# Optimization experiments

Measured on AMD Instinct MI355X. Metric: run time of the kernel, lower is better.

## Reference

```python
import jax, jax.numpy as jnp
import numpy as np

D_MODEL, D_STATE, EXPAND = 1024, 256, 2
BATCH, SEQ = 8, 2048


def setup_inputs() -> dict:
    key = jax.random.key(0)
    ks = jax.random.split(key, 7)
    s = 0.02
    return {
        "x": jax.random.normal(ks[0], (BATCH, SEQ, D_MODEL), jnp.float32),
        "W_in": jax.random.normal(ks[1], (D_MODEL, D_MODEL * EXPAND), jnp.float32) * s,
        "b_in": jax.random.normal(ks[2], (D_MODEL * EXPAND,), jnp.float32) * s,
        "W_state": jax.random.normal(ks[3], (D_MODEL * EXPAND, D_STATE), jnp.float32) * s,
        "b_state": jax.random.normal(ks[4], (D_STATE,), jnp.float32) * s,
        "W_out": jax.random.normal(ks[5], (D_STATE, D_MODEL), jnp.float32) * s,
        "b_out": jax.random.normal(ks[6], (D_MODEL,), jnp.float32) * s,
        "init_state": jnp.zeros((1, D_STATE), jnp.float32),
    }


def reference(x, W_in, b_in, W_state, b_state, W_out, b_out, init_state):
    # x: [B, T, D]
    x_proj = jax.nn.silu(jnp.einsum("btd,de->bte", x, W_in) + b_in)  # [B,T,2D]
    # state_proj depends only on x_proj, so batch the GEMM over all timesteps
    updates = jnp.einsum("bte,es->bts", x_proj, W_state) + b_state    # [B,T,S]
    updates_t = jnp.swapaxes(updates, 0, 1)                            # [T,B,S]
    state0 = jnp.broadcast_to(init_state, (x.shape[0], init_state.shape[1]))

    def step(state, u):
        new = jax.nn.silu(state + u)
        return new, new

    _, states = jax.lax.scan(step, state0, updates_t)  # [T,B,S]
    out = jnp.einsum("tbs,sd->tbd", states, W_out) + b_out  # [T,B,D]
    return jnp.swapaxes(out, 0, 1)  # [B,T,D]
```

## Files before the change

kernel.cpp:

```cpp
#include <hip/hip_runtime.h>
#include <cstdint>
#include <cstddef>

#define BATCH 8
#define SEQ   2048
#define DM    1024
#define DE    2048
#define DSZ   256
#define MROWS (BATCH*SEQ)
#define MCHUNK 8192

typedef _Float16 f16;
typedef _Float16 f16x4 __attribute__((ext_vector_type(4)));
typedef _Float16 f16x8 __attribute__((ext_vector_type(8)));
typedef float  f32x4  __attribute__((ext_vector_type(4)));

__device__ __forceinline__ void glds16(const void* gp, void* lp) {
  __builtin_amdgcn_global_load_lds(
      (const __attribute__((address_space(1))) void*)gp,
      (__attribute__((address_space(3))) void*)lp, 16, 0, 0);
}

__device__ __forceinline__ float silu_f(float x) {
  return x * __builtin_amdgcn_rcpf(1.0f + __expf(-x));
}

__global__ void split_x_k(const float* __restrict__ in, f16* __restrict__ oh,
                          f16* __restrict__ ol, int n) {
  int i = (blockIdx.x * blockDim.x + threadIdx.x) * 4;
  const int stride = gridDim.x * blockDim.x * 4;
  for (; i < n; i += stride) {
    float4 v = *(const float4*)(in + i);
    f16x4 h, l;
    h[0] = (f16)v.x; l[0] = (f16)(v.x - (float)h[0]);
    h[1] = (f16)v.y; l[1] = (f16)(v.y - (float)h[1]);
    h[2] = (f16)v.z; l[2] = (f16)(v.z - (float)h[2]);
    h[3] = (f16)v.w; l[3] = (f16)(v.w - (float)h[3]);
    *(f16x4*)(oh + i) = h;
    *(f16x4*)(ol + i) = l;
  }
}

__global__ void transpose_split_k(const float* __restrict__ in, f16* __restrict__ oh,
                                  f16* __restrict__ ol, int R, int C) {
  __shared__ float tile[32][33];
  const int c0 = blockIdx.x * 32, r0 = blockIdx.y * 32;
  const int tx = threadIdx.x, ty = threadIdx.y;
  #pragma unroll
  for (int i = 0; i < 4; ++i)
    tile[ty + i*8][tx] = in[(size_t)(r0 + ty + i*8) * C + c0 + tx];
  __syncthreads();
  #pragma unroll
  for (int i = 0; i < 4; ++i) {
    float v = tile[tx][ty + i*8];
    f16 h = (f16)v;
    size_t idx = (size_t)(c0 + ty + i*8) * R + r0 + tx;
    oh[idx] = h;
    ol[idx] = (f16)(v - (float)h);
  }
}

__global__ void transpose_cast_f16_k(const float* __restrict__ in, f16* __restrict__ out, int R, int C) {
  __shared__ float tile[32][33];
  const int c0 = blockIdx.x * 32, r0 = blockIdx.y * 32;
  const int tx = threadIdx.x, ty = threadIdx.y;
  #pragma unroll
  for (int i = 0; i < 4; ++i)
    tile[ty + i*8][tx] = in[(size_t)(r0 + ty + i*8) * C + c0 + tx];
  __syncthreads();
  #pragma unroll
  for (int i = 0; i < 4; ++i)
    out[(size_t)(c0 + ty + i*8) * R + r0 + tx] = (f16)tile[tx][ty + i*8];
}

__global__ __launch_bounds__(512) void gemm1_k(const f16* __restrict__ Ah, const f16* __restrict__ Al,
                                               const f16* __restrict__ Bh, const f16* __restrict__ Bl,
                                               const float* __restrict__ bias,
                                               f16* __restrict__ Ch, f16* __restrict__ Cl) {
  const int K = 1024, N = 2048;
  __shared__ f16 sAh[4096], sAl[4096], sBh[4096], sBl[4096];

  const int tid = threadIdx.x;
  const int w = tid >> 6, l = tid & 63;
  const int bid = blockIdx.x;
  const int xcd = bid & 7, loc = bid >> 3;
  const int mt = xcd * 8 + (loc & 7);
  const int nt = loc >> 3;
  const int bm = mt * 128, bn = nt * 128;
  const int wm = (w >> 2) * 64, wn = (w & 3) * 32;
  const int lr = l & 15, lq = l >> 4;

  const int r = tid >> 2, k8 = tid & 3;
  const f16* pAh = Ah + (size_t)(bm + r) * K + k8 * 8;
  const f16* pAl = Al + (size_t)(bm + r) * K + k8 * 8;
  const f16* pBh = Bh + (size_t)(bn + r) * K + k8 * 8;
  const f16* pBl = Bl + (size_t)(bn + r) * K + k8 * 8;
  f16* dAh = sAh + tid * 8; f16* dAl = sAl + tid * 8;
  f16* dBh = sBh + tid * 8; f16* dBl = sBl + tid * 8;

  int offA[4], offB[2];
  #pragma unroll
  for (int i = 0; i < 4; ++i) offA[i] = (wm + i*16 + lr) * 32 + lq * 8;
  #pragma unroll
  for (int j = 0; j < 2; ++j) offB[j] = (wn + j*16 + lr) * 32 + lq * 8;

  f32x4 acc[4][2] = {};

  for (int kk = 0; kk < K; kk += 32) {
    __syncthreads();
    glds16(pAh, dAh); glds16(pAl, dAl);
    glds16(pBh, dBh); glds16(pBl, dBl);
    pAh += 32; pAl += 32; pBh += 32; pBl += 32;
    asm volatile("s_waitcnt vmcnt(0)" ::: "memory");
    __syncthreads();

    f16x8 ah[4], al[4], bh[2], bl[2];
    #pragma unroll
    for (int i = 0; i < 4; ++i) {
      ah[i] = *(const f16x8*)(sAh + offA[i]);
      al[i] = *(const f16x8*)(sAl + offA[i]);
    }
    #pragma unroll
    for (int j = 0; j < 2; ++j) {
      bh[j] = *(const f16x8*)(sBh + offB[j]);
      bl[j] = *(const f16x8*)(sBl + offB[j]);
    }
    #pragma unroll
    for (int i = 0; i < 4; ++i)
      #pragma unroll
      for (int j = 0; j < 2; ++j) {
        acc[i][j] = __builtin_amdgcn_mfma_f32_16x16x32_f16(ah[i], bh[j], acc[i][j], 0, 0, 0);
        acc[i][j] = __builtin_amdgcn_mfma_f32_16x16x32_f16(ah[i], bl[j], acc[i][j], 0, 0, 0);
        acc[i][j] = __builtin_amdgcn_mfma_f32_16x16x32_f16(al[i], bh[j], acc[i][j], 0, 0, 0);
      }
  }

  #pragma unroll
  for (int j = 0; j < 2; ++j) {
    const int col = bn + wn + j*16 + lr;
    const float bv = bias[col];
    #pragma unroll
    for (int i = 0; i < 4; ++i)
      #pragma unroll
      for (int r4 = 0; r4 < 4; ++r4) {
        const int row = bm + wm + i*16 + lq*4 + r4;
        const float s = silu_f(acc[i][j][r4] + bv);
        const f16 h = (f16)s;
        const size_t idx = (size_t)row * N + col;
        Ch[idx] = h;
        Cl[idx] = (f16)(s - (float)h);
      }
  }
}

__global__ __launch_bounds__(256) void gemm2s_k(const f16* __restrict__ Ah, const f16* __restrict__ Al,
                                                const f16* __restrict__ Bh, const f16* __restrict__ Bl,
                                                const float* __restrict__ bias,
                                                float* __restrict__ C) {
  const int K = 2048, N = 256;
  __shared__ f16 sAh[2048], sAl[2048], sBh[4096], sBl[4096];

  const int tid = threadIdx.x;
  const int w = tid >> 6, l = tid & 63;
  const int bm = blockIdx.y * 64, bn = blockIdx.x * 128;
  const int wm = (w & 1) * 32, wn = (w >> 1) * 64;
  const int lr = l & 15, lq = l >> 4;

  const int rA = tid >> 2, k8 = tid & 3;
  const f16* pAh = Ah + (size_t)(bm + rA) * K + k8 * 8;
  const f16* pAl = Al + (size_t)(bm + rA) * K + k8 * 8;
  f16* dAh = sAh + tid * 8; f16* dAl = sAl + tid * 8;
  const f16 *pBh[2], *pBl[2]; f16 *dBh[2], *dBl[2];
  #pragma unroll
  for (int p = 0; p < 2; ++p) {
    const int c = p * 256 + tid;
    const int rB = c >> 2;
    pBh[p] = Bh + (size_t)(bn + rB) * K + (c & 3) * 8;
    pBl[p] = Bl + (size_t)(bn + rB) * K + (c & 3) * 8;
    dBh[p] = sBh + (size_t)c * 8; dBl[p] = sBl + (size_t)c * 8;
  }

  int offA[2], offB[4];
  #pragma unroll
  for (int i = 0; i < 2; ++i) offA[i] = (wm + i*16 + lr) * 32 + lq * 8;
  #pragma unroll
  for (int j = 0; j < 4; ++j) offB[j] = (wn + j*16 + lr) * 32 + lq * 8;

  f32x4 acc[2][4] = {};

  for (int kk = 0; kk < K; kk += 32) {
    __syncthreads();
    glds16(pAh, dAh); glds16(pAl, dAl);
    pAh += 32; pAl += 32;
    #pragma unroll
    for (int p = 0; p < 2; ++p) {
      glds16(pBh[p], dBh[p]); pBh[p] += 32;
      glds16(pBl[p], dBl[p]); pBl[p] += 32;
    }
    asm volatile("s_waitcnt vmcnt(0)" ::: "memory");
    __syncthreads();

    f16x8 ah[2], al[2], bh[4], bl[4];
    #pragma unroll
    for (int i = 0; i < 2; ++i) {
      ah[i] = *(const f16x8*)(sAh + offA[i]);
      al[i] = *(const f16x8*)(sAl + offA[i]);
    }
    #pragma unroll
    for (int j = 0; j < 4; ++j) {
      bh[j] = *(const f16x8*)(sBh + offB[j]);
      bl[j] = *(const f16x8*)(sBl + offB[j]);
    }
    #pragma unroll
    for (int i = 0; i < 2; ++i)
      #pragma unroll
      for (int j = 0; j < 4; ++j) {
        acc[i][j] = __builtin_amdgcn_mfma_f32_16x16x32_f16(ah[i], bh[j], acc[i][j], 0, 0, 0);
        acc[i][j] = __builtin_amdgcn_mfma_f32_16x16x32_f16(ah[i], bl[j], acc[i][j], 0, 0, 0);
        acc[i][j] = __builtin_amdgcn_mfma_f32_16x16x32_f16(al[i], bh[j], acc[i][j], 0, 0, 0);
      }
  }

  #pragma unroll
  for (int j = 0; j < 4; ++j) {
    const int col = bn + wn + j*16 + lr;
    const float bv = bias[col];
    #pragma unroll
    for (int i = 0; i < 2; ++i)
      #pragma unroll
      for (int r4 = 0; r4 < 4; ++r4) {
        const int row = bm + wm + i*16 + lq*4 + r4;
        C[(size_t)row * N + col] = acc[i][j][r4] + bv;
      }
  }
}

__global__ __launch_bounds__(256) void gemm3_k(const f16* __restrict__ A,
                                               const f16* __restrict__ Bt,
                                               const float* __restrict__ bias,
                                               float* __restrict__ C) {
  const int K = 256, N = 1024;
  __shared__ f16 sA[4096], sB[4096];

  const int tid = threadIdx.x;
  const int w = tid >> 6, l = tid & 63;
  const int bm = blockIdx.y * 128, bn = blockIdx.x * 128;
  const int wm = (w >> 1) * 64, wn = (w & 1) * 64;
  const int lr = l & 15, lq = l >> 4;

  const f16 *pA[2], *pB[2]; f16 *dA[2], *dB[2];
  #pragma unroll
  for (int p = 0; p < 2; ++p) {
    const int c = p * 256 + tid;
    const int r = c >> 2, k8 = c & 3;
    pA[p] = A  + (size_t)(bm + r) * K + k8 * 8;
    pB[p] = Bt + (size_t)(bn + r) * K + k8 * 8;
    dA[p] = sA + (size_t)c * 8;
    dB[p] = sB + (size_t)c * 8;
  }

  int offA[4], offB[4];
  #pragma unroll
  for (int i = 0; i < 4; ++i) {
    offA[i] = (wm + i*16 + lr) * 32 + lq * 8;
    offB[i] = (wn + i*16 + lr) * 32 + lq * 8;
  }

  f32x4 acc[4][4] = {};

  for (int kk = 0; kk < K; kk += 32) {
    __syncthreads();
    glds16(pA[0], dA[0]); glds16(pA[1], dA[1]);
    glds16(pB[0], dB[0]); glds16(pB[1], dB[1]);
    pA[0] += 32; pA[1] += 32; pB[0] += 32; pB[1] += 32;
    asm volatile("s_waitcnt vmcnt(0)" ::: "memory");
    __syncthreads();

    f16x8 af[4], bfr[4];
    #pragma unroll
    for (int i = 0; i < 4; ++i) af[i]  = *(const f16x8*)(sA + offA[i]);
    #pragma unroll
    for (int j = 0; j < 4; ++j) bfr[j] = *(const f16x8*)(sB + offB[j]);
    #pragma unroll
    for (int i = 0; i < 4; ++i)
      #pragma unroll
      for (int j = 0; j < 4; ++j)
        acc[i][j] = __builtin_amdgcn_mfma_f32_16x16x32_f16(af[i], bfr[j], acc[i][j], 0, 0, 0);
  }

  #pragma unroll
  for (int j = 0; j < 4; ++j) {
    const int col = bn + wn + j*16 + lr;
    const float bv = bias[col];
    #pragma unroll
    for (int i = 0; i < 4; ++i)
      #pragma unroll
      for (int r4 = 0; r4 < 4; ++r4) {
        const int row = bm + wm + i*16 + lq*4 + r4;
        C[(size_t)row * N + col] = acc[i][j][r4] + bv;
      }
  }
}

#define L2E 1.4426950408889634f
__global__ void scan_k(const float* __restrict__ upd, const float* __restrict__ init,
                       f16* __restrict__ states) {
  const int b = blockIdx.x, s = threadIdx.x;
  const float* u = upd + (size_t)b * SEQ * DSZ + s;
  f16* st = states + (size_t)b * SEQ * DSZ + s;
  float state = init[s];

  float ucur[16], unext[16], ulog[16];
  #pragma unroll
  for (int i = 0; i < 16; ++i) ucur[i] = u[(size_t)i * DSZ];
  #pragma unroll
  for (int i = 0; i < 16; ++i) ulog[i] = ucur[i] * (-L2E);

  for (int t0 = 0; t0 < SEQ; t0 += 16) {
    if (t0 + 16 < SEQ) {
      #pragma unroll
      for (int i = 0; i < 16; ++i) unext[i] = u[(size_t)(t0 + 16 + i) * DSZ];
    }
    f16 res[16];
    #pragma unroll
    for (int i = 0; i < 16; ++i) {
      const float e = __builtin_amdgcn_exp2f(__builtin_fmaf(state, -L2E, ulog[i]));
      const float x = state + ucur[i];
      state = x * __builtin_amdgcn_rcpf(1.0f + e);
      res[i] = (f16)state;
    }
    #pragma unroll
    for (int i = 0; i < 16; ++i) st[(size_t)(t0 + i) * DSZ] = res[i];
    #pragma unroll
    for (int i = 0; i < 16; ++i) { ucur[i] = unext[i]; ulog[i] = unext[i] * (-L2E); }
  }
}

extern "C" void kernel_launch(void* const* d_in, const int* in_sizes, int n_in,
                              void* d_out, int out_size, void* d_ws, size_t ws_size,
                              hipStream_t stream) {
  const float* x       = (const float*)d_in[0];
  const float* W_in    = (const float*)d_in[1];
  const float* b_in    = (const float*)d_in[2];
  const float* W_state = (const float*)d_in[3];
  const float* b_state = (const float*)d_in[4];
  const float* W_out   = (const float*)d_in[5];
  const float* b_out   = (const float*)d_in[6];
  const float* init_st = (const float*)d_in[7];
  float* out = (float*)d_out;

  char* ws = (char*)d_ws;
  f16*   xh        = (f16*)(ws + 0);
  f16*   xl        = (f16*)(ws + 33554432);
  f16*   xproj_h   = (f16*)(ws + 67108864);
  f16*   xproj_l   = (f16*)(ws + 100663296);
  float* upd       = (float*)(ws + 134217728);
  f16*   states    = (f16*)(ws + 150994944);
  f16*   w_in_h    = (f16*)(ws + 159383552);
  f16*   w_in_l    = (f16*)(ws + 163577856);
  f16*   w_state_h = (f16*)(ws + 167772160);
  f16*   w_state_l = (f16*)(ws + 168820736);
  f16*   w_out_t   = (f16*)(ws + 169869312);

  split_x_k<<<4096, 256, 0, stream>>>(x, xh, xl, MROWS * DM);
  dim3 tb(32, 8);
  transpose_split_k<<<dim3(DE/32,  DM/32), tb, 0, stream>>>(W_in,    w_in_h,    w_in_l,    DM,  DE);
  transpose_split_k<<<dim3(DSZ/32, DE/32), tb, 0, stream>>>(W_state, w_state_h, w_state_l, DE,  DSZ);
  transpose_cast_f16_k<<<dim3(DM/32, DSZ/32), tb, 0, stream>>>(W_out, w_out_t, DSZ, DM);

  for (int c = 0; c < 2; ++c) {
    const size_t ro = (size_t)c * MCHUNK;
    gemm1_k<<<1024, 512, 0, stream>>>(
        xh + ro * DM, xl + ro * DM, w_in_h, w_in_l, b_in, xproj_h, xproj_l);
    gemm2s_k<<<dim3(DSZ/128, MCHUNK/64), 256, 0, stream>>>(
        xproj_h, xproj_l, w_state_h, w_state_l, b_state, upd + ro * DSZ);
  }

  scan_k<<<BATCH, DSZ, 0, stream>>>(upd, init_st, states);

  gemm3_k<<<dim3(DM/128, MROWS/128), 256, 0, stream>>>(states, w_out_t, b_out, out);
}
```

Baseline: 625.4 us.

## Swizzle LDS tiles, shrink gemm2 tile, split scan across more blocks

Applies an XOR swizzle to the k-chunk index of the LDS tiles in all three GEMMs, so fragment reads hit different LDS banks. gemm2s moves from a 64x128 to a 64x64 tile, doubling the grid to raise occupancy. The scan kernel is split into 32 blocks of 64 threads instead of 8 blocks of 256, and now prefetches two chunks ahead to hide load latency. The trade-offs are more registers in the scan and more redundant A-tile reloads in gemm2s.

Result: faster. 592.6 us (-5.2%).

```diff
diff --git a/kernel.cpp b/kernel.cpp
--- a/kernel.cpp
+++ b/kernel.cpp
@@ -24,6 +24,8 @@
 __device__ __forceinline__ float silu_f(float x) {
   return x * __builtin_amdgcn_rcpf(1.0f + __expf(-x));
 }
+
+__device__ __forceinline__ int swz(int k8, int r) { return k8 ^ ((r >> 1) & 3); }
 
 __global__ void split_x_k(const float* __restrict__ in, f16* __restrict__ oh,
                           f16* __restrict__ ol, int n) {
@@ -90,7 +92,7 @@
   const int wm = (w >> 2) * 64, wn = (w & 3) * 32;
   const int lr = l & 15, lq = l >> 4;
 
-  const int r = tid >> 2, k8 = tid & 3;
+  const int r = tid >> 2, k8 = swz(tid & 3, r);
   const f16* pAh = Ah + (size_t)(bm + r) * K + k8 * 8;
   const f16* pAl = Al + (size_t)(bm + r) * K + k8 * 8;
   const f16* pBh = Bh + (size_t)(bn + r) * K + k8 * 8;
@@ -100,9 +102,15 @@
 
   int offA[4], offB[2];
   #pragma unroll
-  for (int i = 0; i < 4; ++i) offA[i] = (wm + i*16 + lr) * 32 + lq * 8;
-  #pragma unroll
-  for (int j = 0; j < 2; ++j) offB[j] = (wn + j*16 + lr) * 32 + lq * 8;
+  for (int i = 0; i < 4; ++i) {
+    const int row = wm + i*16 + lr;
+    offA[i] = row * 32 + swz(lq, row) * 8;
+  }
+  #pragma unroll
+  for (int j = 0; j < 2; ++j) {
+    const int row = wn + j*16 + lr;
+    offB[j] = row * 32 + swz(lq, row) * 8;
+  }
 
   f32x4 acc[4][2] = {};
 
@@ -158,63 +166,59 @@
                                                 const float* __restrict__ bias,
                                                 float* __restrict__ C) {
   const int K = 2048, N = 256;
-  __shared__ f16 sAh[2048], sAl[2048], sBh[4096], sBl[4096];
+  __shared__ f16 sAh[2048], sAl[2048], sBh[2048], sBl[2048];
 
   const int tid = threadIdx.x;
   const int w = tid >> 6, l = tid & 63;
-  const int bm = blockIdx.y * 64, bn = blockIdx.x * 128;
-  const int wm = (w & 1) * 32, wn = (w >> 1) * 64;
+  const int bm = blockIdx.y * 64, bn = blockIdx.x * 64;
+  const int wm = (w & 1) * 32, wn = (w >> 1) * 32;
   const int lr = l & 15, lq = l >> 4;
 
-  const int rA = tid >> 2, k8 = tid & 3;
-  const f16* pAh = Ah + (size_t)(bm + rA) * K + k8 * 8;
-  const f16* pAl = Al + (size_t)(bm + rA) * K + k8 * 8;
+  const int r = tid >> 2, k8 = swz(tid & 3, r);
+  const f16* pAh = Ah + (size_t)(bm + r) * K + k8 * 8;
+  const f16* pAl = Al + (size_t)(bm + r) * K + k8 * 8;
+  const f16* pBh = Bh + (size_t)(bn + r) * K + k8 * 8;
+  const f16* pBl = Bl + (size_t)(bn + r) * K + k8 * 8;
   f16* dAh = sAh + tid * 8; f16* dAl = sAl + tid * 8;
-  const f16 *pBh[2], *pBl[2]; f16 *dBh[2], *dBl[2];
-  #pragma unroll
-  for (int p = 0; p < 2; ++p) {
-    const int c = p * 256 + tid;
-    const int rB = c >> 2;
-    pBh[p] = Bh + (size_t)(bn + rB) * K + (c & 3) * 8;
-    pBl[p] = Bl + (size_t)(bn + rB) * K + (c & 3) * 8;
-    dBh[p] = sBh + (size_t)c * 8; dBl[p] = sBl + (size_t)c * 8;
-  }
-
-  int offA[2], offB[4];
-  #pragma unroll
-  for (int i = 0; i < 2; ++i) offA[i] = (wm + i*16 + lr) * 32 + lq * 8;
-  #pragma unroll
-  for (int j = 0; j < 4; ++j) offB[j] = (wn + j*16 + lr) * 32 + lq * 8;
-
-  f32x4 acc[2][4] = {};
+  f16* dBh = sBh + tid * 8; f16* dBl = sBl + tid * 8;
+
+  int offA[2], offB[2];
+  #pragma unroll
+  for (int i = 0; i < 2; ++i) {
+    const int row = wm + i*16 + lr;
+    offA[i] = row * 32 + swz(lq, row) * 8;
+  }
+  #pragma unroll
+  for (int j = 0; j < 2; ++j) {
+    const int row = wn + j*16 + lr;
+    offB[j] = row * 32 + swz(lq, row) * 8;
+  }
+
+  f32x4 acc[2][2] = {};
 
   for (int kk = 0; kk < K; kk += 32) {
     __syncthreads();
     glds16(pAh, dAh); glds16(pAl, dAl);
-    pAh += 32; pAl += 32;
-    #pragma unroll
-    for (int p = 0; p < 2; ++p) {
-      glds16(pBh[p], dBh[p]); pBh[p] += 32;
-      glds16(pBl[p], dBl[p]); pBl[p] += 32;
-    }
+    glds16(pBh, dBh); glds16(pBl, dBl);
+    pAh += 32; pAl += 32; pBh += 32; pBl += 32;
     asm volatile("s_waitcnt vmcnt(0)" ::: "memory");
     __syncthreads();
 
-    f16x8 ah[2], al[2], bh[4], bl[4];
+    f16x8 ah[2], al[2], bh[2], bl[2];
     #pragma unroll
     for (int i = 0; i < 2; ++i) {
       ah[i] = *(const f16x8*)(sAh + offA[i]);
       al[i] = *(const f16x8*)(sAl + offA[i]);
     }
     #pragma unroll
-    for (int j = 0; j < 4; ++j) {
+    for (int j = 0; j < 2; ++j) {
       bh[j] = *(const f16x8*)(sBh + offB[j]);
       bl[j] = *(const f16x8*)(sBl + offB[j]);
     }
     #pragma unroll
     for (int i = 0; i < 2; ++i)
       #pragma unroll
-      for (int j = 0; j < 4; ++j) {
+      for (int j = 0; j < 2; ++j) {
         acc[i][j] = __builtin_amdgcn_mfma_f32_16x16x32_f16(ah[i], bh[j], acc[i][j], 0, 0, 0);
         acc[i][j] = __builtin_amdgcn_mfma_f32_16x16x32_f16(ah[i], bl[j], acc[i][j], 0, 0, 0);
         acc[i][j] = __builtin_amdgcn_mfma_f32_16x16x32_f16(al[i], bh[j], acc[i][j], 0, 0, 0);
@@ -222,7 +226,7 @@
   }
 
   #pragma unroll
-  for (int j = 0; j < 4; ++j) {
+  for (int j = 0; j < 2; ++j) {
     const int col = bn + wn + j*16 + lr;
     const float bv = bias[col];
     #pragma unroll
@@ -252,7 +256,7 @@
   #pragma unroll
   for (int p = 0; p < 2; ++p) {
     const int c = p * 256 + tid;
-    const int r = c >> 2, k8 = c & 3;
+    const int r = c >> 2, k8 = swz(c & 3, r);
     pA[p] = A  + (size_t)(bm + r) * K + k8 * 8;
     pB[p] = Bt + (size_t)(bn + r) * K + k8 * 8;
     dA[p] = sA + (size_t)c * 8;
@@ -262,8 +266,10 @@
   int offA[4], offB[4];
   #pragma unroll
   for (int i = 0; i < 4; ++i) {
-    offA[i] = (wm + i*16 + lr) * 32 + lq * 8;
-    offB[i] = (wn + i*16 + lr) * 32 + lq * 8;
+    const int rowA = wm + i*16 + lr;
+    const int rowB = wn + i*16 + lr;
+    offA[i] = rowA * 32 + swz(lq, rowA) * 8;
+    offB[i] = rowB * 32 + swz(lq, rowB) * 8;
   }
 
   f32x4 acc[4][4] = {};
@@ -303,36 +309,40 @@
 }
 
 #define L2E 1.4426950408889634f
-__global__ void scan_k(const float* __restrict__ upd, const float* __restrict__ init,
-                       f16* __restrict__ states) {
-  const int b = blockIdx.x, s = threadIdx.x;
+__global__ __launch_bounds__(64) void scan_k(const float* __restrict__ upd,
+                                             const float* __restrict__ init,
+                                             f16* __restrict__ states) {
+  const int b = blockIdx.x >> 2, sq = blockIdx.x & 3;
+  const int s = sq * 64 + threadIdx.x;
   const float* u = upd + (size_t)b * SEQ * DSZ + s;
   f16* st = states + (size_t)b * SEQ * DSZ + s;
   float state = init[s];
 
-  float ucur[16], unext[16], ulog[16];
-  #pragma unroll
-  for (int i = 0; i < 16; ++i) ucur[i] = u[(size_t)i * DSZ];
-  #pragma unroll
-  for (int i = 0; i < 16; ++i) ulog[i] = ucur[i] * (-L2E);
+  float r0[16], r1[16], r2[16], ulog[16];
+  #pragma unroll
+  for (int i = 0; i < 16; ++i) r0[i] = u[(size_t)i * DSZ];
+  #pragma unroll
+  for (int i = 0; i < 16; ++i) r1[i] = u[(size_t)(16 + i) * DSZ];
+  #pragma unroll
+  for (int i = 0; i < 16; ++i) ulog[i] = r0[i] * (-L2E);
 
   for (int t0 = 0; t0 < SEQ; t0 += 16) {
-    if (t0 + 16 < SEQ) {
-      #pragma unroll
-      for (int i = 0; i < 16; ++i) unext[i] = u[(size_t)(t0 + 16 + i) * DSZ];
+    if (t0 + 32 < SEQ) {
+      #pragma unroll
+      for (int i = 0; i < 16; ++i) r2[i] = u[(size_t)(t0 + 32 + i) * DSZ];
     }
     f16 res[16];
     #pragma unroll
     for (int i = 0; i < 16; ++i) {
       const float e = __builtin_amdgcn_exp2f(__builtin_fmaf(state, -L2E, ulog[i]));
-      const float x = state + ucur[i];
+      const float x = state + r0[i];
       state = x * __builtin_amdgcn_rcpf(1.0f + e);
       res[i] = (f16)state;
     }
     #pragma unroll
     for (int i = 0; i < 16; ++i) st[(size_t)(t0 + i) * DSZ] = res[i];
     #pragma unroll
-    for (int i = 0; i < 16; ++i) { ucur[i] = unext[i]; ulog[i] = unext[i] * (-L2E); }
+    for (int i = 0; i < 16; ++i) { r0[i] = r1[i]; ulog[i] = r1[i] * (-L2E); r1[i] = r2[i]; }
   }
 }
 
@@ -372,11 +382,11 @@
     const size_t ro = (size_t)c * MCHUNK;
     gemm1_k<<<1024, 512, 0, stream>>>(
         xh + ro * DM, xl + ro * DM, w_in_h, w_in_l, b_in, xproj_h, xproj_l);
-    gemm2s_k<<<dim3(DSZ/128, MCHUNK/64), 256, 0, stream>>>(
+    gemm2s_k<<<dim3(DSZ/64, MCHUNK/64), 256, 0, stream>>>(
         xproj_h, xproj_l, w_state_h, w_state_l, b_state, upd + ro * DSZ);
   }
 
-  scan_k<<<BATCH, DSZ, 0, stream>>>(upd, init_st, states);
+  scan_k<<<BATCH*4, 64, 0, stream>>>(upd, init_st, states);
 
   gemm3_k<<<dim3(DM/128, MROWS/128), 256, 0, stream>>>(states, w_out_t, b_out, out);
 }
```
